# Optimization experiments

Hardware: AMD Instinct MI355X
Metric: run time of the kernel (lower is better)

The kernel has to match this reference:

```python
import jax, jax.numpy as jnp
import numpy as np

HID = 3584; NH = 16; NKV = 8; HD = 256; S = 3072; WIN = 2048
SOFTCAP = 50.0; QSCALE = 256.0 ** -0.5  # query_pre_attn_scalar = 256
NEG = -2.3819763e38


def _rope(x, cos, sin):
    # x: (B, S, heads, HD); cos/sin: (S, HD//2). Gemma half-split complex RoPE.
    x1, x2 = jnp.split(x, 2, axis=-1)
    c = cos[None, :, None, :]
    s = sin[None, :, None, :]
    return jnp.concatenate([x1 * c - x2 * s, x1 * s + x2 * c], axis=-1)


def setup_inputs() -> dict:
    key = jax.random.key(0)
    k1, k2, k3 = jax.random.split(key, 3)
    hidden_states = jax.random.normal(k1, (1, S, HID), jnp.float32)
    qkv_w = jax.random.normal(k2, (NH * HD + 2 * NKV * HD, HID), jnp.float32) * 0.02
    o_w = jax.random.normal(k3, (HID, NH * HD), jnp.float32) * 0.02
    inv = 1.0 / (10000.0 ** (jnp.arange(0, HD, 2, dtype=jnp.float32) / HD))
    ang = jnp.arange(S, dtype=jnp.float32)[:, None] * inv[None, :]
    freqs_cis = jnp.stack([jnp.cos(ang), jnp.sin(ang)], axis=-1)  # (S, HD//2, 2)
    kv_write_indices = jnp.arange(S, dtype=jnp.int32)
    k_cache = jnp.zeros((1, S, NKV, HD), jnp.float32)
    v_cache = jnp.zeros((1, S, NKV, HD), jnp.float32)
    i = jnp.arange(S)[:, None]
    j = jnp.arange(S)[None, :]
    mask = jnp.where(j <= i, 0.0, NEG).astype(jnp.float32)[None, None]  # causal (1,1,S,S)
    return dict(hidden_states=hidden_states, freqs_cis=freqs_cis,
                kv_write_indices=kv_write_indices, k_cache=k_cache, v_cache=v_cache,
                mask=mask, qkv_w=qkv_w, o_w=o_w)


def reference(hidden_states, freqs_cis, kv_write_indices, k_cache, v_cache, mask, qkv_w, o_w):
    B, L, _ = hidden_states.shape
    qkv = hidden_states @ qkv_w.T  # (B, L, 8192)
    xq, xk, xv = jnp.split(qkv, [NH * HD, NH * HD + NKV * HD], axis=-1)
    xq = xq.reshape(B, L, NH, HD)
    xk = xk.reshape(B, L, NKV, HD)
    xv = xv.reshape(B, L, NKV, HD)
    cos, sin = freqs_cis[..., 0], freqs_cis[..., 1]
    xq = _rope(xq, cos, sin)
    xk = _rope(xk, cos, sin)
    # KV cache index_copy_ on dim 1
    k_all = k_cache.at[:, kv_write_indices].set(xk)  # (B, T, NKV, HD)
    v_all = v_cache.at[:, kv_write_indices].set(xv)
    T = k_all.shape[1]
    G = NH // NKV  # queries per kv head; grouped einsum avoids repeat_interleave
    q = (xq * QSCALE).transpose(0, 2, 1, 3).reshape(B, NKV, G, L, HD)
    k = k_all.transpose(0, 2, 1, 3)  # (B, NKV, T, HD)
    v = v_all.transpose(0, 2, 1, 3)
    scores = jnp.einsum('bkgsd,bktd->bkgst', q, k)
    # logit softcapping
    scores = jnp.tanh(scores / SOFTCAP) * SOFTCAP
    # sliding-window band applied on top of the provided (causal) mask
    i = jnp.arange(L)[:, None]
    j = jnp.arange(T)[None, :]
    band = (j >= i - WIN + 1) & (j <= i + WIN - 1)
    m = jnp.where(band, mask, NEG)  # (1,1,L,T)
    scores = scores + m[:, :, None]  # broadcast over group dim
    probs = jax.nn.softmax(scores.astype(jnp.float32), axis=-1).astype(q.dtype)
    out = jnp.einsum('bkgst,bktd->bkgsd', probs, v)
    out = out.reshape(B, NH, L, HD).transpose(0, 2, 1, 3).reshape(B, L, NH * HD)
    return out @ o_w.T
```

## Files before the change

kernel.cpp:

```cpp
#include <hip/hip_runtime.h>

#define S_LEN 3072
#define NHQ 16
#define NKVH 8
#define HDIM 256
#define WIN 2048
#define QKV_COLS 8192

typedef __bf16 bf16x8 __attribute__((ext_vector_type(8)));
typedef float f32x4 __attribute__((ext_vector_type(4)));
typedef float f32x16 __attribute__((ext_vector_type(16)));

__device__ __forceinline__ unsigned short f2bf(float f) {
    union { float f; unsigned u; } v; v.f = f;
    unsigned r = v.u + 0x7FFFu + ((v.u >> 16) & 1u);
    return (unsigned short)(r >> 16);
}
__device__ __forceinline__ float bf2f(unsigned short u) {
    union { unsigned u; float f; } v; v.u = ((unsigned)u) << 16; return v.f;
}

typedef __attribute__((address_space(3))) void lds_void_t;
typedef const __attribute__((address_space(1))) void glb_void_t;
__device__ __forceinline__ void async16(const void* g, void* l) {
    __builtin_amdgcn_global_load_lds((glb_void_t*)g, (lds_void_t*)l, 16, 0, 0);
}

__global__ __launch_bounds__(256) void cast_bf16_kernel(const float* __restrict__ src,
                                                        unsigned short* __restrict__ dst,
                                                        int n) {
    int i = (blockIdx.x * 256 + threadIdx.x) * 4;
    if (i >= n) return;
    float4 v = *(const float4*)(src + i);
    ushort4 o;
    o.x = f2bf(v.x); o.y = f2bf(v.y); o.z = f2bf(v.z); o.w = f2bf(v.w);
    *(ushort4*)(dst + i) = o;
}

template <int OUT_BF16>
__global__ __launch_bounds__(256) void gemm_bt(const unsigned short* __restrict__ A,
                                               const unsigned short* __restrict__ B,
                                               void* __restrict__ Cv,
                                               int N, int K) {
    __shared__ __align__(16) unsigned short At[3][128 * 32];
    __shared__ __align__(16) unsigned short Bt[3][128 * 32];
    const int tid = threadIdx.x;
    const int wid = tid >> 6, lane = tid & 63;
    const int ln = lane & 15, quad = lane >> 4;

    int bm, bn;
    {
        const int nwg = gridDim.x * gridDim.y;
        int orig = blockIdx.y * gridDim.x + blockIdx.x;
        int wg = orig;
        if ((nwg & 7) == 0) {
            const int cpx = nwg >> 3;
            wg = (orig & 7) * cpx + (orig >> 3);
        }
        bm = wg / gridDim.x;
        bn = wg % gridDim.x;
    }
    const int wm = wid >> 1, wn = wid & 1;

    const f32x4 fzero = {0.f, 0.f, 0.f, 0.f};
    f32x4 acc[4][4];
#pragma unroll
    for (int i = 0; i < 4; i++) {
#pragma unroll
        for (int j = 0; j < 4; j++) acc[i][j] = fzero;
    }

    const unsigned short* gA = A + (size_t)(bm * 128 + wid * 32 + (lane >> 2)) * K + (lane & 3) * 8;
    const unsigned short* gB = B + (size_t)(bn * 128 + wid * 32 + (lane >> 2)) * K + (lane & 3) * 8;
    const int lbase = wid * 32 * 32;

    auto STAGE = [&](int k0, int b) {
        async16(gA + k0,          &At[b][lbase]);
        async16(gA + k0 + 16 * K, &At[b][lbase + 16 * 32]);
        async16(gB + k0,          &Bt[b][lbase]);
        async16(gB + k0 + 16 * K, &Bt[b][lbase + 16 * 32]);
    };

    const int NT = K >> 5;
    STAGE(0, 0);
    STAGE(32, 1);
    int rb = 0;

    for (int t = 0; t < NT; ++t) {
        if (t + 1 < NT) { asm volatile("s_waitcnt vmcnt(4)" ::: "memory"); }
        else            { asm volatile("s_waitcnt vmcnt(0)" ::: "memory"); }
        __builtin_amdgcn_s_barrier();
        asm volatile("" ::: "memory");

        if (t + 2 < NT) {
            const int wb = (rb >= 1) ? rb - 1 : 2;
            STAGE((t + 2) * 32, wb);
        }

        bf16x8 af[4], bfr[4];
#pragma unroll
        for (int mt = 0; mt < 4; mt++)
            af[mt] = *(const bf16x8*)(&At[rb][(wm * 64 + mt * 16 + ln) * 32 + quad * 8]);
#pragma unroll
        for (int nt = 0; nt < 4; nt++)
            bfr[nt] = *(const bf16x8*)(&Bt[rb][(wn * 64 + nt * 16 + ln) * 32 + quad * 8]);
#pragma unroll
        for (int mt = 0; mt < 4; mt++) {
#pragma unroll
            for (int nt = 0; nt < 4; nt++)
                acc[mt][nt] = __builtin_amdgcn_mfma_f32_16x16x32_bf16(af[mt], bfr[nt], acc[mt][nt], 0, 0, 0);
        }
        rb = (rb >= 2) ? 0 : rb + 1;
    }

    const int row0 = bm * 128 + wm * 64 + quad * 4;
    const int col0 = bn * 128 + wn * 64 + ln;
    if (OUT_BF16) {
        unsigned short* C = (unsigned short*)Cv;
#pragma unroll
        for (int mt = 0; mt < 4; mt++) {
#pragma unroll
            for (int nt = 0; nt < 4; nt++) {
#pragma unroll
                for (int rr = 0; rr < 4; rr++)
                    C[(size_t)(row0 + mt * 16 + rr) * N + col0 + nt * 16] = f2bf(acc[mt][nt][rr]);
            }
        }
    } else {
        float* C = (float*)Cv;
#pragma unroll
        for (int mt = 0; mt < 4; mt++) {
#pragma unroll
            for (int nt = 0; nt < 4; nt++) {
#pragma unroll
                for (int rr = 0; rr < 4; rr++)
                    C[(size_t)(row0 + mt * 16 + rr) * N + col0 + nt * 16] = acc[mt][nt][rr];
            }
        }
    }
}

__global__ __launch_bounds__(256) void rope_kernel(const unsigned short* __restrict__ qkv,
                                                   const float* __restrict__ freqs,
                                                   const int* __restrict__ kvidx,
                                                   unsigned short* __restrict__ Qb,
                                                   unsigned short* __restrict__ Kb) {
    int t = blockIdx.x * 256 + threadIdx.x;
    int d = t & 127;
    int t2 = t >> 7;
    int hh = t2 % 24;
    int pos = t2 / 24;
    if (pos >= S_LEN) return;
    float2 cs = *(const float2*)(freqs + ((size_t)pos * 128 + d) * 2);
    if (hh < NHQ) {
        const unsigned short* src = qkv + (size_t)pos * QKV_COLS + hh * HDIM + d;
        float x1 = bf2f(src[0]), x2 = bf2f(src[128]);
        float o1 = (x1 * cs.x - x2 * cs.y) * 0.0625f;
        float o2 = (x1 * cs.y + x2 * cs.x) * 0.0625f;
        unsigned short* dst = Qb + ((size_t)hh * S_LEN + pos) * HDIM + d;
        dst[0] = f2bf(o1);
        dst[128] = f2bf(o2);
    } else {
        int kvh = hh - NHQ;
        const unsigned short* src = qkv + (size_t)pos * QKV_COLS + NHQ * HDIM + kvh * HDIM + d;
        float x1 = bf2f(src[0]), x2 = bf2f(src[128]);
        float o1 = x1 * cs.x - x2 * cs.y;
        float o2 = x1 * cs.y + x2 * cs.x;
        int wpos = kvidx[pos];
        unsigned short* dst = Kb + ((size_t)kvh * S_LEN + wpos) * HDIM + d;
        dst[0] = f2bf(o1);
        dst[128] = f2bf(o2);
    }
}

__global__ __launch_bounds__(256) void vtrans_kernel(const unsigned short* __restrict__ qkv,
                                                     const int* __restrict__ kvidx,
                                                     unsigned short* __restrict__ Vbt) {
    __shared__ unsigned short T[64][72];
    int pos0 = blockIdx.x * 64;
    int c0 = blockIdx.y * 64;
    int a = threadIdx.x >> 6;
    int b = threadIdx.x & 63;
#pragma unroll
    for (int r = 0; r < 16; r++) {
        int pl = r * 4 + a;
        T[pl][b] = qkv[(size_t)(pos0 + pl) * QKV_COLS + 6144 + c0 + b];
    }
    __syncthreads();
    int wpos = kvidx[pos0 + b];
#pragma unroll
    for (int r = 0; r < 16; r++) {
        int cl = r * 4 + a;
        Vbt[(size_t)(c0 + cl) * S_LEN + wpos] = T[b][cl];
    }
}

__global__ __launch_bounds__(256, 1) void attn_kernel(const unsigned short* __restrict__ Qb,
                                                      const unsigned short* __restrict__ Kb,
                                                      const unsigned short* __restrict__ Vbt,
                                                      unsigned short* __restrict__ attn_out) {
    __shared__ __align__(16) unsigned short Kl[3][32 * 256];
    __shared__ __align__(16) unsigned short Vl[3][256 * 32];
    __shared__ __align__(16) unsigned short Plb[4][1024];

    const int h = blockIdx.x & 15;
    const int qb = 23 - (blockIdx.x >> 4);

    const int kv = h >> 1;
    const int q0 = qb * 128;
    const int tid = threadIdx.x;
    const int wid = tid >> 6, lane = tid & 63;
    const int ln32 = lane & 31, hi = lane >> 5;
    const int qw0 = q0 + wid * 32;

    bf16x8 qf[16];
    {
        const unsigned short* qrow = Qb + ((size_t)h * S_LEN + qw0 + ln32) * HDIM + hi * 8;
#pragma unroll
        for (int s = 0; s < 16; s++)
            qf[s] = *(const bf16x8*)(qrow + s * 16);
    }

    f32x16 pacc[8];
#pragma unroll
    for (int dt = 0; dt < 8; dt++) {
#pragma unroll
        for (int i = 0; i < 16; i++) pacc[dt][i] = 0.f;
    }
    float ps[16];
#pragma unroll
    for (int r = 0; r < 16; r++) ps[r] = 0.f;

    const int imin = qw0;
    const int imax = qw0 + 31;

    const int t_lo = (q0 >= WIN) ? ((q0 - (WIN - 1)) >> 5) : 0;
    const int t_hi = (q0 + 127) >> 5;
    const int ts = t_lo;
    const int te = t_hi + 1;

    const unsigned short* kSrcA = Kb + ((size_t)kv * S_LEN + (tid >> 5)) * HDIM
                                  + ((tid & 31) ^ ((tid >> 5) & 7)) * 8;
    const unsigned short* vSrcA = Vbt + ((size_t)kv * HDIM + (tid >> 2)) * S_LEN
                                  + ((tid & 3) ^ ((tid >> 3) & 3)) * 8;

    auto STAGE = [&](int tile, int b) {
        const int p0x = tile * 32;
        const unsigned short* ksg = kSrcA + (size_t)p0x * HDIM;
        const unsigned short* vsg = vSrcA + p0x;
#pragma unroll
        for (int c = 0; c < 4; c++)
            async16(ksg + (size_t)(c * 8) * HDIM, &Kl[b][(c * 256 + tid) * 8]);
#pragma unroll
        for (int c = 0; c < 4; c++)
            async16(vsg + (size_t)(c * 64) * S_LEN, &Vl[b][(c * 256 + tid) * 8]);
    };

    STAGE(ts, 0);
    STAGE(ts + 1, 1);

    unsigned short* plw = &Plb[wid][0];
    const int kswz = ln32 & 7;
    int rb = 0;

    for (int tt = ts; tt < te; tt++) {
        if (tt + 1 < te) { asm volatile("s_waitcnt vmcnt(8)" ::: "memory"); }
        else             { asm volatile("s_waitcnt vmcnt(0)" ::: "memory"); }
        __builtin_amdgcn_s_barrier();
        asm volatile("" ::: "memory");

        if (tt + 2 < te) {
            const int wb = (rb >= 1) ? rb - 1 : 2;
            STAGE(tt + 2, wb);
        }

        const int p0 = tt * 32;
        const bool live = (p0 <= imax) && (p0 + 31 >= imin - WIN + 1);
        if (live) {
            const unsigned short* kb = Kl[rb];
            f32x16 sacc;
#pragma unroll
            for (int i = 0; i < 16; i++) sacc[i] = 0.f;
#pragma unroll
            for (int s = 0; s < 16; s++) {
                bf16x8 kf = *(const bf16x8*)(kb + ln32 * 256 + ((((s << 1) + hi) ^ kswz) << 3));
                sacc = __builtin_amdgcn_mfma_f32_32x32x16_bf16(qf[s], kf, sacc, 0, 0, 0);
            }

            const bool full = (p0 + 31 <= imin) && (p0 >= imax - WIN + 1);
#pragma unroll
            for (int r = 0; r < 16; r++) {
                float z = __expf(sacc[r] * 0.04f);
                float t = fmaf(-100.f, __builtin_amdgcn_rcpf(z + 1.f), 50.f);
                float p = __expf(t);
                const int qloc = (r & 3) + 8 * (r >> 2) + 4 * hi;
                if (!full) {
                    const int i = qw0 + qloc;
                    const int j = p0 + ln32;
                    p = ((j <= i) && (j + WIN > i)) ? p : 0.f;
                }
                ps[r] += p;
                plw[qloc * 32 + (((ln32 >> 3) ^ ((qloc >> 1) & 3)) << 3) + (ln32 & 7)] = f2bf(p);
            }

            bf16x8 pa0 = *(const bf16x8*)(plw + ln32 * 32 + ((hi ^ ((ln32 >> 1) & 3)) << 3));
            bf16x8 pa1 = *(const bf16x8*)(plw + ln32 * 32 + (((2 + hi) ^ ((ln32 >> 1) & 3)) << 3));
            const unsigned short* vb = Vl[rb];
#pragma unroll
            for (int dt = 0; dt < 8; dt++) {
                const int d = dt * 32 + ln32;
                const int vswz = (d >> 1) & 3;
                bf16x8 v0 = *(const bf16x8*)(vb + d * 32 + ((hi ^ vswz) << 3));
                pacc[dt] = __builtin_amdgcn_mfma_f32_32x32x16_bf16(pa0, v0, pacc[dt], 0, 0, 0);
                bf16x8 v1 = *(const bf16x8*)(vb + d * 32 + (((2 + hi) ^ vswz) << 3));
                pacc[dt] = __builtin_amdgcn_mfma_f32_32x32x16_bf16(pa1, v1, pacc[dt], 0, 0, 0);
            }
        }
        rb = (rb >= 2) ? 0 : rb + 1;
    }

#pragma unroll
    for (int r = 0; r < 16; r++) {
        float s = ps[r];
#pragma unroll
        for (int o = 1; o <= 16; o <<= 1)
            s += __shfl_xor(s, o);
        ps[r] = s;
    }

#pragma unroll
    for (int dt = 0; dt < 8; dt++) {
#pragma unroll
        for (int r = 0; r < 16; r++) {
            const int q = qw0 + (r & 3) + 8 * (r >> 2) + 4 * hi;
            float o = pacc[dt][r] * __builtin_amdgcn_rcpf(ps[r]);
            attn_out[(size_t)q * 4096 + h * HDIM + dt * 32 + ln32] = f2bf(o);
        }
    }
}

extern "C" void kernel_launch(void* const* d_in, const int* in_sizes, int n_in,
                              void* d_out, int out_size, void* d_ws, size_t ws_size,
                              hipStream_t stream) {
    (void)in_sizes; (void)n_in; (void)out_size; (void)ws_size;
    const float* hidden = (const float*)d_in[0];
    const float* freqs  = (const float*)d_in[1];
    const int* kvidx    = (const int*)d_in[2];
    const float* qkv_w  = (const float*)d_in[6];
    const float* o_w    = (const float*)d_in[7];
    float* out = (float*)d_out;

    char* ws = (char*)d_ws;
    unsigned short* hs_bf   = (unsigned short*)(ws);
    unsigned short* w1_bf   = (unsigned short*)(ws + 22020096);
    unsigned short* w2_bf   = (unsigned short*)(ws + 80740352);
    unsigned short* qkv_bf  = (unsigned short*)(ws + 110100480);
    unsigned short* Qb      = (unsigned short*)(ws + 160432128);
    unsigned short* Kb      = (unsigned short*)(ws + 185597952);
    unsigned short* Vbt     = (unsigned short*)(ws + 198180864);
    unsigned short* attn_bf = (unsigned short*)(ws + 210763776);

    cast_bf16_kernel<<<10752, 256, 0, stream>>>(hidden, hs_bf, 11010048);
    cast_bf16_kernel<<<28672, 256, 0, stream>>>(qkv_w, w1_bf, 29360128);
    cast_bf16_kernel<<<14336, 256, 0, stream>>>(o_w, w2_bf, 14680064);

    gemm_bt<1><<<dim3(64, 24), 256, 0, stream>>>(hs_bf, w1_bf, (void*)qkv_bf, 8192, 3584);

    rope_kernel<<<36864, 256, 0, stream>>>(qkv_bf, freqs, kvidx, Qb, Kb);
    vtrans_kernel<<<dim3(48, 32), 256, 0, stream>>>(qkv_bf, kvidx, Vbt);

    attn_kernel<<<384, 256, 0, stream>>>(Qb, Kb, Vbt, attn_bf);

    gemm_bt<0><<<dim3(28, 24), 256, 0, stream>>>(attn_bf, w2_bf, (void*)out, 3584, 4096);
}
```

Baseline: 874.4 us.

## Enlarge GEMM tiles to 256x256 with 512 threads and swizzled LDS

Rewrites the bf16 GEMM to use 256x256 block tiles with K-step 64, 8 waves each computing 128x64, double-buffered async LDS loads with an XOR swizzle to avoid bank conflicts, and raised MFMA priority. The larger tile raises arithmetic intensity and cuts global/LDS traffic per FLOP. In exchange, grids shrink to 384 and 168 blocks, which risks poor wave quantization and idle CUs on the output projection, and LDS use limits occupancy.

```diff
diff --git a/kernel.cpp b/kernel.cpp
--- a/kernel.cpp
+++ b/kernel.cpp
@@ -38,15 +38,16 @@
 }
 
 template <int OUT_BF16>
-__global__ __launch_bounds__(256) void gemm_bt(const unsigned short* __restrict__ A,
-                                               const unsigned short* __restrict__ B,
-                                               void* __restrict__ Cv,
-                                               int N, int K) {
-    __shared__ __align__(16) unsigned short At[3][128 * 32];
-    __shared__ __align__(16) unsigned short Bt[3][128 * 32];
+__global__ __launch_bounds__(512, 2) void gemm_bt(const unsigned short* __restrict__ A,
+                                                  const unsigned short* __restrict__ B,
+                                                  void* __restrict__ Cv,
+                                                  int N, int K) {
+    __shared__ __align__(16) unsigned short Al[2][256 * 64];
+    __shared__ __align__(16) unsigned short Bl[2][256 * 64];
     const int tid = threadIdx.x;
     const int wid = tid >> 6, lane = tid & 63;
     const int ln = lane & 15, quad = lane >> 4;
+    const int wm = wid >> 2, wn = wid & 3;
 
     int bm, bn;
     {
@@ -60,65 +61,71 @@
         bm = wg / gridDim.x;
         bn = wg % gridDim.x;
     }
-    const int wm = wid >> 1, wn = wid & 1;
 
     const f32x4 fzero = {0.f, 0.f, 0.f, 0.f};
-    f32x4 acc[4][4];
-#pragma unroll
-    for (int i = 0; i < 4; i++) {
+    f32x4 acc[8][4];
+#pragma unroll
+    for (int i = 0; i < 8; i++) {
 #pragma unroll
         for (int j = 0; j < 4; j++) acc[i][j] = fzero;
     }
 
-    const unsigned short* gA = A + (size_t)(bm * 128 + wid * 32 + (lane >> 2)) * K + (lane & 3) * 8;
-    const unsigned short* gB = B + (size_t)(bn * 128 + wid * 32 + (lane >> 2)) * K + (lane & 3) * 8;
-    const int lbase = wid * 32 * 32;
+    const unsigned short* gA = A + (size_t)(bm * 256 + (tid >> 3)) * K
+                               + (((tid & 7) ^ ((tid >> 3) & 7)) * 8);
+    const unsigned short* gB = B + (size_t)(bn * 256 + (tid >> 3)) * K
+                               + (((tid & 7) ^ ((tid >> 3) & 7)) * 8);
 
     auto STAGE = [&](int k0, int b) {
-        async16(gA + k0,          &At[b][lbase]);
-        async16(gA + k0 + 16 * K, &At[b][lbase + 16 * 32]);
-        async16(gB + k0,          &Bt[b][lbase]);
-        async16(gB + k0 + 16 * K, &Bt[b][lbase + 16 * 32]);
+#pragma unroll
+        for (int c = 0; c < 4; c++)
+            async16(gA + (size_t)(c * 64) * K + k0, &Al[b][(c * 512 + tid) * 8]);
+#pragma unroll
+        for (int c = 0; c < 4; c++)
+            async16(gB + (size_t)(c * 64) * K + k0, &Bl[b][(c * 512 + tid) * 8]);
     };
 
-    const int NT = K >> 5;
+    const int NT = K >> 6;
     STAGE(0, 0);
-    STAGE(32, 1);
     int rb = 0;
+    const int aswz = ln & 7;
 
     for (int t = 0; t < NT; ++t) {
-        if (t + 1 < NT) { asm volatile("s_waitcnt vmcnt(4)" ::: "memory"); }
-        else            { asm volatile("s_waitcnt vmcnt(0)" ::: "memory"); }
+        asm volatile("s_waitcnt vmcnt(0)" ::: "memory");
         __builtin_amdgcn_s_barrier();
         asm volatile("" ::: "memory");
 
-        if (t + 2 < NT) {
-            const int wb = (rb >= 1) ? rb - 1 : 2;
-            STAGE((t + 2) * 32, wb);
-        }
-
-        bf16x8 af[4], bfr[4];
-#pragma unroll
-        for (int mt = 0; mt < 4; mt++)
-            af[mt] = *(const bf16x8*)(&At[rb][(wm * 64 + mt * 16 + ln) * 32 + quad * 8]);
-#pragma unroll
-        for (int nt = 0; nt < 4; nt++)
-            bfr[nt] = *(const bf16x8*)(&Bt[rb][(wn * 64 + nt * 16 + ln) * 32 + quad * 8]);
-#pragma unroll
-        for (int mt = 0; mt < 4; mt++) {
+        if (t + 1 < NT) STAGE((t + 1) << 6, rb ^ 1);
+
+        const unsigned short* al = Al[rb];
+        const unsigned short* bl = Bl[rb];
+#pragma unroll
+        for (int h = 0; h < 2; ++h) {
+            const int cs = ((h * 4 + quad) ^ aswz) * 8;
+            bf16x8 af[8], bfr[4];
+#pragma unroll
+            for (int mt = 0; mt < 8; mt++)
+                af[mt] = *(const bf16x8*)(al + (wm * 128 + mt * 16 + ln) * 64 + cs);
 #pragma unroll
             for (int nt = 0; nt < 4; nt++)
-                acc[mt][nt] = __builtin_amdgcn_mfma_f32_16x16x32_bf16(af[mt], bfr[nt], acc[mt][nt], 0, 0, 0);
-        }
-        rb = (rb >= 2) ? 0 : rb + 1;
-    }
-
-    const int row0 = bm * 128 + wm * 64 + quad * 4;
-    const int col0 = bn * 128 + wn * 64 + ln;
+                bfr[nt] = *(const bf16x8*)(bl + (wn * 64 + nt * 16 + ln) * 64 + cs);
+            __builtin_amdgcn_s_setprio(1);
+#pragma unroll
+            for (int mt = 0; mt < 8; mt++) {
+#pragma unroll
+                for (int nt = 0; nt < 4; nt++)
+                    acc[mt][nt] = __builtin_amdgcn_mfma_f32_16x16x32_bf16(af[mt], bfr[nt], acc[mt][nt], 0, 0, 0);
+            }
+            __builtin_amdgcn_s_setprio(0);
+        }
+        rb ^= 1;
+    }
+
+    const int row0 = bm * 256 + wm * 128 + quad * 4;
+    const int col0 = bn * 256 + wn * 64 + ln;
     if (OUT_BF16) {
         unsigned short* C = (unsigned short*)Cv;
 #pragma unroll
-        for (int mt = 0; mt < 4; mt++) {
+        for (int mt = 0; mt < 8; mt++) {
 #pragma unroll
             for (int nt = 0; nt < 4; nt++) {
 #pragma unroll
@@ -129,7 +136,7 @@
     } else {
         float* C = (float*)Cv;
 #pragma unroll
-        for (int mt = 0; mt < 4; mt++) {
+        for (int mt = 0; mt < 8; mt++) {
 #pragma unroll
             for (int nt = 0; nt < 4; nt++) {
 #pragma unroll
@@ -364,12 +371,12 @@
     cast_bf16_kernel<<<28672, 256, 0, stream>>>(qkv_w, w1_bf, 29360128);
     cast_bf16_kernel<<<14336, 256, 0, stream>>>(o_w, w2_bf, 14680064);
 
-    gemm_bt<1><<<dim3(64, 24), 256, 0, stream>>>(hs_bf, w1_bf, (void*)qkv_bf, 8192, 3584);
+    gemm_bt<1><<<dim3(32, 12), 512, 0, stream>>>(hs_bf, w1_bf, (void*)qkv_bf, 8192, 3584);
 
     rope_kernel<<<36864, 256, 0, stream>>>(qkv_bf, freqs, kvidx, Qb, Kb);
     vtrans_kernel<<<dim3(48, 32), 256, 0, stream>>>(qkv_bf, kvidx, Vbt);
 
     attn_kernel<<<384, 256, 0, stream>>>(Qb, Kb, Vbt, attn_bf);
 
-    gemm_bt<0><<<dim3(28, 24), 256, 0, stream>>>(attn_bf, w2_bf, (void*)out, 3584, 4096);
-}
+    gemm_bt<0><<<dim3(14, 12), 512, 0, stream>>>(attn_bf, w2_bf, (void*)out, 3584, 4096);
+}
```

Result: slower. 918.0 us (+5.0%).
